# Kernel tuning notes

Hardware: AMD Instinct MI355X
Metric: run time of the kernel (lower is better)

Reference implementation:

```python
import jax, jax.numpy as jnp
import numpy as np

GAMMA = 0.99
LMBDA = 0.95
SHAPE = (8192, 256, 4, 1)  # (batch, steps, agents, 1)


def setup_inputs() -> dict:
    key = jax.random.key(0)
    k1, k2, k3, k4 = jax.random.split(key, 4)
    reward = jax.random.normal(k1, SHAPE, dtype=jnp.float32)
    # sparse binary termination flags (as float, matching terminated.float())
    terminated = (jax.random.uniform(k2, SHAPE) < 0.01).astype(jnp.float32)
    value = jax.random.normal(k3, SHAPE, dtype=jnp.float32)
    next_value = jax.random.normal(k4, SHAPE, dtype=jnp.float32)
    return {"reward": reward, "terminated": terminated,
            "value": value, "next_value": next_value}


def _gae(reward, terminated, value, next_value):
    not_done = 1.0 - terminated
    # delta_t = r_t + gamma * V(s_{t+1}) * not_done_t - V(s_t), all steps at once
    delta = reward + GAMMA * next_value * not_done - value  # (B, T, ...)

    # time-major for the scan: (T, B, ...)
    delta_t = jnp.moveaxis(delta, 1, 0)
    nd_t = jnp.moveaxis(not_done, 1, 0)

    def step(gae, x):
        d, nd = x
        gae = d + GAMMA * LMBDA * nd * gae
        return gae, gae

    init = jnp.zeros(delta_t.shape[1:], dtype=delta.dtype)
    # reverse=True: backward-time recurrence, outputs aligned to original order
    _, adv_t = jax.lax.scan(step, init, (delta_t, nd_t), reverse=True)
    advantages = jnp.moveaxis(adv_t, 0, 1)  # back to (B, T, ...)
    returns = advantages + value
    return advantages, returns


def reference(reward, terminated, value, next_value):
    return _gae(reward, terminated, value, next_value)
```

## Files before the change

### kernel.cpp

```cpp
#include <hip/hip_runtime.h>


#define GAMMA 0.99f
#define LMBDA 0.95f

constexpr int T = 256;
constexpr int A = 4;

__global__ __launch_bounds__(256) void gae_scan_kernel(
    const float* __restrict__ reward,
    const float* __restrict__ terminated,
    const float* __restrict__ value,
    const float* __restrict__ next_value,
    float* __restrict__ adv_out,
    float* __restrict__ ret_out)
{
    const int b = blockIdx.x;
    const int i = threadIdx.x;
    const int t = T - 1 - i;
    const int idx = b * T + t;

    const float4 r  = ((const float4*)reward)[idx];
    const float4 tm = ((const float4*)terminated)[idx];
    const float4 v  = ((const float4*)value)[idx];
    const float4 nv = ((const float4*)next_value)[idx];

    float vv[4] = {v.x, v.y, v.z, v.w};
    float d[4], k[4];
    {
        float rr[4] = {r.x, r.y, r.z, r.w};
        float tt[4] = {tm.x, tm.y, tm.z, tm.w};
        float nn[4] = {nv.x, nv.y, nv.z, nv.w};
#pragma unroll
        for (int c = 0; c < 4; ++c) {
            float nd = 1.0f - tt[c];
            d[c] = rr[c] + GAMMA * nn[c] * nd - vv[c];
            k[c] = GAMMA * LMBDA * nd;
        }
    }

    const int lane = i & 63;
    const int wave = i >> 6;

#pragma unroll
    for (int off = 1; off < 64; off <<= 1) {
        float pd[4], pk[4];
#pragma unroll
        for (int c = 0; c < 4; ++c) {
            pd[c] = __shfl_up(d[c], (unsigned)off, 64);
            pk[c] = __shfl_up(k[c], (unsigned)off, 64);
        }
        if (lane >= off) {
#pragma unroll
            for (int c = 0; c < 4; ++c) {
                d[c] = d[c] + k[c] * pd[c];
                k[c] = k[c] * pk[c];
            }
        }
    }

    __shared__ float aggD[4][4];
    __shared__ float aggK[4][4];
    if (lane == 63) {
#pragma unroll
        for (int c = 0; c < 4; ++c) { aggD[wave][c] = d[c]; aggK[wave][c] = k[c]; }
    }
    __syncthreads();

    float Dp[4] = {0.f, 0.f, 0.f, 0.f};
    for (int w = 0; w < wave; ++w) {
#pragma unroll
        for (int c = 0; c < 4; ++c) {
            Dp[c] = aggD[w][c] + aggK[w][c] * Dp[c];
        }
    }

    float g[4];
#pragma unroll
    for (int c = 0; c < 4; ++c) g[c] = d[c] + k[c] * Dp[c];

    ((float4*)adv_out)[idx] = make_float4(g[0], g[1], g[2], g[3]);
    ((float4*)ret_out)[idx] = make_float4(g[0] + vv[0], g[1] + vv[1],
                                          g[2] + vv[2], g[3] + vv[3]);
}

extern "C" void kernel_launch(void* const* d_in, const int* in_sizes, int n_in,
                              void* d_out, int out_size, void* d_ws, size_t ws_size,
                              hipStream_t stream) {
    const float* reward     = (const float*)d_in[0];
    const float* terminated = (const float*)d_in[1];
    const float* value      = (const float*)d_in[2];
    const float* next_value = (const float*)d_in[3];

    const int B = 8192;
    const int n_elem = B * T * A;
    float* adv = (float*)d_out;
    float* ret = adv + n_elem;

    gae_scan_kernel<<<B, 256, 0, stream>>>(reward, terminated, value,
                                           next_value, adv, ret);
}
```

Measured before the change: 179.9 us.

## Map one batch row per wavefront with serial per-lane chunks and shuffle scan

Reassigns work so each 64-lane wavefront handles one batch row, with each lane owning 16 consecutive timesteps of one agent. Lanes do a serial local scan, then a short cross-lane shuffle scan over chunk aggregates, then a serial fix-up pass that writes outputs. This removes shared memory, the block barrier and most shuffle traffic, and raises per-thread memory parallelism, at the cost of more registers and scalar instead of float4 accesses.

Measured after the change: 211.6 us. 1.18x slower.

```diff
diff --git a/kernel.cpp b/kernel.cpp
--- a/kernel.cpp
+++ b/kernel.cpp
@@ -5,9 +5,8 @@
 #define LMBDA 0.95f
 
 constexpr int T = 256;
-constexpr int A = 4;
 
-__global__ __launch_bounds__(256) void gae_scan_kernel(
+__global__ __launch_bounds__(256, 4) void gae_scan_kernel(
     const float* __restrict__ reward,
     const float* __restrict__ terminated,
     const float* __restrict__ value,
@@ -15,73 +14,49 @@
     float* __restrict__ adv_out,
     float* __restrict__ ret_out)
 {
-    const int b = blockIdx.x;
-    const int i = threadIdx.x;
-    const int t = T - 1 - i;
-    const int idx = b * T + t;
+    const int lane = threadIdx.x & 63;
+    const int b    = (blockIdx.x * blockDim.x + threadIdx.x) >> 6;
+    const int tc   = lane >> 2;
+    const int a    = lane & 3;
 
-    const float4 r  = ((const float4*)reward)[idx];
-    const float4 tm = ((const float4*)terminated)[idx];
-    const float4 v  = ((const float4*)value)[idx];
-    const float4 nv = ((const float4*)next_value)[idx];
+    const int base = b * 1024 + 1020 - 64 * tc + a;
 
-    float vv[4] = {v.x, v.y, v.z, v.w};
-    float d[4], k[4];
-    {
-        float rr[4] = {r.x, r.y, r.z, r.w};
-        float tt[4] = {tm.x, tm.y, tm.z, tm.w};
-        float nn[4] = {nv.x, nv.y, nv.z, nv.w};
+    float d[16], c[16], vv[16];
 #pragma unroll
-        for (int c = 0; c < 4; ++c) {
-            float nd = 1.0f - tt[c];
-            d[c] = rr[c] + GAMMA * nn[c] * nd - vv[c];
-            k[c] = GAMMA * LMBDA * nd;
-        }
+    for (int j = 0; j < 16; ++j) {
+        const int o = base - 4 * j;
+        const float r  = reward[o];
+        const float tm = terminated[o];
+        const float v  = value[o];
+        const float nv = next_value[o];
+        const float nd = 1.0f - tm;
+        d[j]  = r + GAMMA * nv * nd - v;
+        c[j]  = (GAMMA * LMBDA) * nd;
+        vv[j] = v;
     }
 
-    const int lane = i & 63;
-    const int wave = i >> 6;
+    float D = d[0], K = c[0];
+#pragma unroll
+    for (int j = 1; j < 16; ++j) { D = d[j] + c[j] * D; K = c[j] * K; }
 
 #pragma unroll
-    for (int off = 1; off < 64; off <<= 1) {
-        float pd[4], pk[4];
-#pragma unroll
-        for (int c = 0; c < 4; ++c) {
-            pd[c] = __shfl_up(d[c], (unsigned)off, 64);
-            pk[c] = __shfl_up(k[c], (unsigned)off, 64);
-        }
-        if (lane >= off) {
-#pragma unroll
-            for (int c = 0; c < 4; ++c) {
-                d[c] = d[c] + k[c] * pd[c];
-                k[c] = k[c] * pk[c];
-            }
-        }
+    for (int s = 1; s < 16; s <<= 1) {
+        const float pD = __shfl_up(D, (unsigned)(s * 4), 64);
+        const float pK = __shfl_up(K, (unsigned)(s * 4), 64);
+        if (tc >= s) { D = D + K * pD; K = K * pK; }
     }
 
-    __shared__ float aggD[4][4];
-    __shared__ float aggK[4][4];
-    if (lane == 63) {
+    float x = __shfl_up(D, 4u, 64);
+    if (tc == 0) x = 0.0f;
+
+    float g = x;
 #pragma unroll
-        for (int c = 0; c < 4; ++c) { aggD[wave][c] = d[c]; aggK[wave][c] = k[c]; }
+    for (int j = 0; j < 16; ++j) {
+        g = d[j] + c[j] * g;
+        const int o = base - 4 * j;
+        adv_out[o] = g;
+        ret_out[o] = g + vv[j];
     }
-    __syncthreads();
-
-    float Dp[4] = {0.f, 0.f, 0.f, 0.f};
-    for (int w = 0; w < wave; ++w) {
-#pragma unroll
-        for (int c = 0; c < 4; ++c) {
-            Dp[c] = aggD[w][c] + aggK[w][c] * Dp[c];
-        }
-    }
-
-    float g[4];
-#pragma unroll
-    for (int c = 0; c < 4; ++c) g[c] = d[c] + k[c] * Dp[c];
-
-    ((float4*)adv_out)[idx] = make_float4(g[0], g[1], g[2], g[3]);
-    ((float4*)ret_out)[idx] = make_float4(g[0] + vv[0], g[1] + vv[1],
-                                          g[2] + vv[2], g[3] + vv[3]);
 }
 
 extern "C" void kernel_launch(void* const* d_in, const int* in_sizes, int n_in,
@@ -93,10 +68,11 @@
     const float* next_value = (const float*)d_in[3];
 
     const int B = 8192;
-    const int n_elem = B * T * A;
+    const int n_elem = B * T * 4;
     float* adv = (float*)d_out;
     float* ret = adv + n_elem;
 
-    gae_scan_kernel<<<B, 256, 0, stream>>>(reward, terminated, value,
-                                           next_value, adv, ret);
+    const int blocks = (B * 64) / 256;
+    gae_scan_kernel<<<blocks, 256, 0, stream>>>(reward, terminated, value,
+                                                next_value, adv, ret);
 }
```
